# Kernel optimization log

Measured on AMD Instinct MI355X. Metric: run time of the kernel, lower is better.

Reference implementation:

```python
import jax, jax.numpy as jnp
import numpy as np

# ---- problem constants (mirror AdjustInstanceArea __init__ args) ----
NUM_NODES = 2_000_000
NUM_MOVABLE = 1_500_000
NUM_FILLER = 400_000
NUM_NETS = 1_500_000
PINS_PER_NET = 4                       # uniform netpin_start = arange(0, P+1, 4)
NUM_PINS = NUM_NETS * PINS_PER_NET
XL, XH, YL, YH = 0.0, 1000.0, 0.0, 1000.0
NBX = NBY = 512
BIN_W = (XH - XL) / NBX
BIN_H = (YH - YL) / NBY
UNIT_H_CAP = 1.5                       # unit horizontal routing capacity
UNIT_V_CAP = 1.5                       # unit vertical routing capacity
MAX_RATE = 2.0                         # max_route_opt_adjust_rate
MIN_RATE = 1.0 / MAX_RATE
EPS = 1e-6


def setup_inputs() -> dict:
    key = jax.random.key(0)
    k = jax.random.split(key, 4)
    x = jax.random.uniform(k[0], (NUM_NODES,), jnp.float32, XL, XH - 4.0)
    y = jax.random.uniform(k[1], (NUM_NODES,), jnp.float32, YL, YH - 4.0)
    pos = jnp.concatenate([x, y])                      # [2*num_nodes], x then y

    # pins clustered around net centers (realistic small net bboxes)
    rng = np.random.default_rng(0)
    centers = rng.uniform(0.0, 1000.0, size=(NUM_NETS, 1, 2)).astype(np.float32)
    jit = rng.uniform(-20.0, 20.0, size=(NUM_NETS, PINS_PER_NET, 2)).astype(np.float32)
    ppos = np.clip(centers + jit, 0.0, 1000.0)         # [nets, pins_per_net, 2], in net order

    # flat_netpin: pin ids grouped by net; pin_pos indexed by pin id
    flat_netpin = rng.permutation(NUM_PINS).astype(np.int32)
    px = np.empty(NUM_PINS, np.float32); py = np.empty(NUM_PINS, np.float32)
    px[flat_netpin] = ppos[..., 0].reshape(-1)
    py[flat_netpin] = ppos[..., 1].reshape(-1)
    pin_pos = jnp.concatenate([jnp.asarray(px), jnp.asarray(py)])  # [2*num_pins]

    pin2net = jnp.asarray(np.repeat(np.arange(NUM_NETS, dtype=np.int32), PINS_PER_NET))

    node_size_x = jax.random.uniform(k[2], (NUM_NODES,), jnp.float32, 1.0, 4.0)
    node_size_y = jax.random.uniform(k[3], (NUM_NODES,), jnp.float32, 1.0, 4.0)
    return {"pos": pos, "pin_pos": pin_pos,
            "node_size_x": node_size_x, "node_size_y": node_size_y,
            "flat_netpin": jnp.asarray(flat_netpin), "pin2net": pin2net}


def _rect_accum(vals, blx, bly, bhx, bhy):
    """Accumulate vals over inclusive bin rectangles via difference map + 2D cumsum."""
    D = jnp.zeros((NBX + 1, NBY + 1), vals.dtype)
    D = D.at[blx, bly].add(vals)
    D = D.at[bhx + 1, bly].add(-vals)
    D = D.at[blx, bhy + 1].add(-vals)
    D = D.at[bhx + 1, bhy + 1].add(vals)
    return jnp.cumsum(jnp.cumsum(D, axis=0), axis=1)[:NBX, :NBY]


def reference(pos, pin_pos, node_size_x, node_size_y, flat_netpin, pin2net):
    # ---- InstanceRouteOptimizationArea: RUDY routing demand per bin ----
    px = pin_pos[:NUM_PINS][flat_netpin].reshape(NUM_NETS, PINS_PER_NET)
    py = pin_pos[NUM_PINS:][flat_netpin].reshape(NUM_NETS, PINS_PER_NET)
    net_xl = jnp.min(px, axis=1); net_xh = jnp.max(px, axis=1)
    net_yl = jnp.min(py, axis=1); net_yh = jnp.max(py, axis=1)
    bw = net_xh - net_xl
    bh = net_yh - net_yl
    barea = jnp.maximum(bw * bh, EPS)
    dens_h = bw / barea                                # horizontal wire density
    dens_v = bh / barea                                # vertical wire density

    blx = jnp.clip(jnp.floor((net_xl - XL) / BIN_W), 0, NBX - 1).astype(jnp.int32)
    bhx = jnp.clip(jnp.floor((net_xh - XL) / BIN_W), 0, NBX - 1).astype(jnp.int32)
    bly = jnp.clip(jnp.floor((net_yl - YL) / BIN_H), 0, NBY - 1).astype(jnp.int32)
    bhy = jnp.clip(jnp.floor((net_yh - YL) / BIN_H), 0, NBY - 1).astype(jnp.int32)

    util_h = _rect_accum(dens_h, blx, bly, bhx, bhy) / UNIT_H_CAP
    util_v = _rect_accum(dens_v, blx, bly, bhx, bhy) / UNIT_V_CAP

    # per-movable-node utilization (gather at node center bin)
    x = pos[:NUM_NODES]; y = pos[NUM_NODES:]
    nsx_m = node_size_x[:NUM_MOVABLE]; nsy_m = node_size_y[:NUM_MOVABLE]
    cx = x[:NUM_MOVABLE] + 0.5 * nsx_m
    cy = y[:NUM_MOVABLE] + 0.5 * nsy_m
    bix = jnp.clip(jnp.floor((cx - XL) / BIN_W), 0, NBX - 1).astype(jnp.int32)
    biy = jnp.clip(jnp.floor((cy - YL) / BIN_H), 0, NBY - 1).astype(jnp.int32)
    util = jnp.maximum(util_h[bix, biy], util_v[bix, biy])
    ratio = jnp.clip(util, MIN_RATE, MAX_RATE)

    area_old = nsx_m * nsy_m
    instance_route_area = area_old * ratio

    # ---- AdjustInstanceArea: rescale under max_total_area budget ----
    filler_area_old = jnp.sum(node_size_x[NUM_NODES - NUM_FILLER:] *
                              node_size_y[NUM_NODES - NUM_FILLER:])
    max_total_area = jnp.sum(area_old) + filler_area_old
    scale = jnp.minimum(1.0, max_total_area / jnp.maximum(jnp.sum(instance_route_area), EPS))
    new_area = instance_route_area * scale
    sr = jnp.sqrt(new_area / jnp.maximum(area_old, EPS))
    nsx_new = nsx_m * sr
    nsy_new = nsy_m * sr

    # keep cell centers fixed while resizing
    x_out = x.at[:NUM_MOVABLE].add(0.5 * (nsx_m - nsx_new))
    y_out = y.at[:NUM_MOVABLE].add(0.5 * (nsy_m - nsy_new))

    # fillers absorb leftover area budget
    fscale = jnp.sqrt(jnp.maximum(max_total_area - jnp.sum(new_area), 0.0) /
                      jnp.maximum(filler_area_old, EPS))
    nsx_out = node_size_x.at[:NUM_MOVABLE].set(nsx_new)
    nsx_out = nsx_out.at[NUM_NODES - NUM_FILLER:].multiply(fscale)
    nsy_out = node_size_y.at[:NUM_MOVABLE].set(nsy_new)
    nsy_out = nsy_out.at[NUM_NODES - NUM_FILLER:].multiply(fscale)

    return jnp.concatenate([x_out, y_out, nsx_out, nsy_out])  # [4*num_nodes]
```

## Files before the change

### kernel.cpp

```cpp
#include <hip/hip_runtime.h>
#include <math.h>

#define N_NODES   2000000
#define N_MOVABLE 1500000
#define N_FILLER  400000
#define N_NETS    1500000
#define N_PINS    (N_NETS * 4)
#define NB        512
#define NT        16
#define TILE      32
#define NBUCKET   (NT * NT)
#define CAP       10240
#define RED_BLOCKS 512

__device__ __forceinline__ int bin_idx(float v) {
    float b = floorf(v / 1.953125f);
    b = fminf(fmaxf(b, 0.0f), 511.0f);
    return (int)b;
}

__global__ void pack_kernel(const float* __restrict__ pin_pos,
                            float2* __restrict__ pp) {
    int i = blockIdx.x * blockDim.x + threadIdx.x;
    if (i >= N_PINS / 4) return;
    float4 a = reinterpret_cast<const float4*>(pin_pos)[i];
    float4 b = reinterpret_cast<const float4*>(pin_pos + N_PINS)[i];
    float4* o = reinterpret_cast<float4*>(pp + 4 * (size_t)i);
    o[0] = make_float4(a.x, b.x, a.y, b.y);
    o[1] = make_float4(a.z, b.z, a.w, b.w);
}

template <bool PACKED>
__global__ __launch_bounds__(1024)
void gather_bin_kernel(const float* __restrict__ pin_pos,
                       const float2* __restrict__ pp,
                       const int*  __restrict__ flat_netpin,
                       float4* __restrict__ slab,
                       unsigned* __restrict__ g_ptr) {
    __shared__ unsigned hist[NBUCKET];
    __shared__ unsigned base[NBUCKET];
    int t = threadIdx.x;
    if (t < NBUCKET) hist[t] = 0;
    __syncthreads();

    int n = blockIdx.x * 1024 + t;
    float4 r = make_float4(0.f, 0.f, 0.f, 0.f);
    int b = 0;
    unsigned rank = 0;
    bool valid = (n < N_NETS);
    if (valid) {
        int4 fp = *reinterpret_cast<const int4*>(flat_netpin + 4 * n);
        float px0, px1, px2, px3, py0, py1, py2, py3;
        if (PACKED) {
            float2 p0 = pp[fp.x], p1 = pp[fp.y], p2 = pp[fp.z], p3 = pp[fp.w];
            px0 = p0.x; py0 = p0.y; px1 = p1.x; py1 = p1.y;
            px2 = p2.x; py2 = p2.y; px3 = p3.x; py3 = p3.y;
        } else {
            px0 = pin_pos[fp.x]; px1 = pin_pos[fp.y];
            px2 = pin_pos[fp.z]; px3 = pin_pos[fp.w];
            py0 = pin_pos[N_PINS + fp.x]; py1 = pin_pos[N_PINS + fp.y];
            py2 = pin_pos[N_PINS + fp.z]; py3 = pin_pos[N_PINS + fp.w];
        }
        float xl = fminf(fminf(px0, px1), fminf(px2, px3));
        float xh = fmaxf(fmaxf(px0, px1), fmaxf(px2, px3));
        float yl = fminf(fminf(py0, py1), fminf(py2, py3));
        float yh = fmaxf(fmaxf(py0, py1), fmaxf(py2, py3));

        float bw = xh - xl, bh = yh - yl;
        float barea = fmaxf(bw * bh, 1e-6f);
        float vh = (bw / barea) * (1.0f / 1.5f);
        float vv = (bh / barea) * (1.0f / 1.5f);

        unsigned blx = bin_idx(xl), bhx = bin_idx(xh);
        unsigned bly = bin_idx(yl), bhy = bin_idx(yh);

        r.x = vh; r.y = vv;
        r.z = __uint_as_float(blx | (bly << 16));
        r.w = __uint_as_float((bhx + 1) | ((bhy + 1) << 16));
        b = (int)((bly >> 5) * NT + (blx >> 5));
        rank = atomicAdd(&hist[b], 1u);
    }
    __syncthreads();
    if (t < NBUCKET) {
        unsigned c = hist[t];
        base[t] = c ? atomicAdd(&g_ptr[t], c) : 0u;
    }
    __syncthreads();
    if (valid) {
        unsigned slot = base[b] + rank;
        if (slot < CAP) slab[(size_t)b * CAP + slot] = r;
    }
}

__global__ __launch_bounds__(256)
void accum_kernel(const float4* __restrict__ slab,
                  const unsigned* __restrict__ g_cnt,
                  float2* __restrict__ Dp) {
    __shared__ float acc[TILE][TILE][2];
    int wg   = blockIdx.x;
    int half = wg & 1;
    int tile = wg >> 1;
    int tx = tile & (NT - 1);
    int ty = tile >> 4;

    for (int i = threadIdx.x; i < TILE * TILE * 2; i += 256)
        ((float*)acc)[i] = 0.0f;
    __syncthreads();

    int x0 = tx * TILE, y0 = ty * TILE;
    for (int dy = -1; dy <= 0; ++dy) {
        int sy = ty + dy; if (sy < 0) continue;
        for (int dx = -1; dx <= 0; ++dx) {
            int sx = tx + dx; if (sx < 0) continue;
            int sb = sy * NT + sx;
            unsigned cnt = min(g_cnt[sb], (unsigned)CAP);
            unsigned lo = half ? cnt / 2 : 0u;
            unsigned hi = half ? cnt : cnt / 2;
            const float4* recs = slab + (size_t)sb * CAP;
            for (unsigned i = lo + threadIdx.x; i < hi; i += 256) {
                float4 r = recs[i];
                unsigned zlo = __float_as_uint(r.z), zhi = __float_as_uint(r.w);
                int ax0 = (int)(zlo & 0xffffu), ay0 = (int)(zlo >> 16);
                int ax1 = (int)(zhi & 0xffffu), ay1 = (int)(zhi >> 16);
                int X0 = ax0 - x0, X1 = ax1 - x0;
                int Y0 = ay0 - y0, Y1 = ay1 - y0;
                bool inX0 = (unsigned)X0 < TILE, inX1 = (unsigned)X1 < TILE;
                bool inY0 = (unsigned)Y0 < TILE, inY1 = (unsigned)Y1 < TILE;
                if (inX0 && inY0) { atomicAdd(&acc[X0][Y0][0],  r.x); atomicAdd(&acc[X0][Y0][1],  r.y); }
                if (inX1 && inY0) { atomicAdd(&acc[X1][Y0][0], -r.x); atomicAdd(&acc[X1][Y0][1], -r.y); }
                if (inX0 && inY1) { atomicAdd(&acc[X0][Y1][0], -r.x); atomicAdd(&acc[X0][Y1][1], -r.y); }
                if (inX1 && inY1) { atomicAdd(&acc[X1][Y1][0],  r.x); atomicAdd(&acc[X1][Y1][1],  r.y); }
            }
        }
    }
    __syncthreads();
    float2* D = Dp + (size_t)half * NB * NB;
    for (int i = threadIdx.x; i < TILE * TILE; i += 256) {
        int X = i >> 5, Y = i & 31;
        D[(size_t)(x0 + X) * NB + (y0 + Y)] = make_float2(acc[X][Y][0], acc[X][Y][1]);
    }
}

__global__ void fb_scatter_kernel(const float4* __restrict__ rec,
                                  float2* __restrict__ Dp) {
    int n = blockIdx.x * blockDim.x + threadIdx.x;
    if (n >= N_NETS) return;
    float4 r = rec[n];
    unsigned zlo = __float_as_uint(r.z), zhi = __float_as_uint(r.w);
    int ax0 = (int)(zlo & 0xffffu), ay0 = (int)(zlo >> 16);
    int ax1 = (int)(zhi & 0xffffu), ay1 = (int)(zhi >> 16);
    if (ax0 < NB && ay0 < NB) { unsafeAtomicAdd(&Dp[ax0 * NB + ay0].x,  r.x); unsafeAtomicAdd(&Dp[ax0 * NB + ay0].y,  r.y); }
    if (ax1 < NB && ay0 < NB) { unsafeAtomicAdd(&Dp[ax1 * NB + ay0].x, -r.x); unsafeAtomicAdd(&Dp[ax1 * NB + ay0].y, -r.y); }
    if (ax0 < NB && ay1 < NB) { unsafeAtomicAdd(&Dp[ax0 * NB + ay1].x, -r.x); unsafeAtomicAdd(&Dp[ax0 * NB + ay1].y, -r.y); }
    if (ax1 < NB && ay1 < NB) { unsafeAtomicAdd(&Dp[ax1 * NB + ay1].x,  r.x); unsafeAtomicAdd(&Dp[ax1 * NB + ay1].y,  r.y); }
}

__global__ void scan_x_kernel(const float2* __restrict__ Dp,
                              float2* __restrict__ S) {
    __shared__ float2 s[NB];
    int y = blockIdx.x;
    int t = threadIdx.x;
    float2 a = Dp[(size_t)t * NB + y];
    float2 b = Dp[(size_t)NB * NB + (size_t)t * NB + y];
    s[t] = make_float2(a.x + b.x, a.y + b.y);
    __syncthreads();
    for (int off = 1; off < NB; off <<= 1) {
        float2 u = s[t];
        if (t >= off) { float2 w = s[t - off]; u.x += w.x; u.y += w.y; }
        __syncthreads();
        s[t] = u;
        __syncthreads();
    }
    S[(size_t)t * NB + y] = s[t];
}

__global__ void scan_y_kernel(float2* __restrict__ S) {
    __shared__ float2 s[NB];
    int x = blockIdx.x;
    int t = threadIdx.x;
    s[t] = S[(size_t)x * NB + t];
    __syncthreads();
    for (int off = 1; off < NB; off <<= 1) {
        float2 u = s[t];
        if (t >= off) { float2 w = s[t - off]; u.x += w.x; u.y += w.y; }
        __syncthreads();
        s[t] = u;
        __syncthreads();
    }
    S[(size_t)x * NB + t] = s[t];
}

__global__ void reduce_kernel(const float* __restrict__ pos,
                              const float* __restrict__ nsx,
                              const float* __restrict__ nsy,
                              const float2* __restrict__ S,
                              double* __restrict__ partials) {
    double a_old = 0.0, a_route = 0.0, a_fill = 0.0;
    int stride = gridDim.x * blockDim.x;
    for (int i = blockIdx.x * blockDim.x + threadIdx.x;
         i < N_MOVABLE + N_FILLER; i += stride) {
        if (i < N_MOVABLE) {
            float sx = nsx[i], sy = nsy[i];
            float cx = pos[i] + 0.5f * sx;
            float cy = pos[N_NODES + i] + 0.5f * sy;
            int bx = bin_idx(cx), by = bin_idx(cy);
            float2 u2 = S[(size_t)bx * NB + by];
            float ratio = fminf(fmaxf(fmaxf(u2.x, u2.y), 0.5f), 2.0f);
            float area = sx * sy;
            a_old += (double)area;
            a_route += (double)(area * ratio);
        } else {
            int j = (N_NODES - N_FILLER) + (i - N_MOVABLE);
            a_fill += (double)(nsx[j] * nsy[j]);
        }
    }
    for (int off = 32; off > 0; off >>= 1) {
        a_old   += __shfl_down(a_old, off);
        a_route += __shfl_down(a_route, off);
        a_fill  += __shfl_down(a_fill, off);
    }
    __shared__ double sd[4][3];
    int wid = threadIdx.x >> 6, lane = threadIdx.x & 63;
    if (lane == 0) { sd[wid][0] = a_old; sd[wid][1] = a_route; sd[wid][2] = a_fill; }
    __syncthreads();
    if (threadIdx.x == 0) {
        double s0 = 0, s1 = 0, s2 = 0;
        for (int w = 0; w < 4; ++w) { s0 += sd[w][0]; s1 += sd[w][1]; s2 += sd[w][2]; }
        partials[blockIdx.x * 3 + 0] = s0;
        partials[blockIdx.x * 3 + 1] = s1;
        partials[blockIdx.x * 3 + 2] = s2;
    }
}

__global__ void finish_kernel(const double* __restrict__ partials,
                              double* __restrict__ sums) {
    int t = threadIdx.x;
    double s0 = partials[t * 3 + 0];
    double s1 = partials[t * 3 + 1];
    double s2 = partials[t * 3 + 2];
    for (int off = 32; off > 0; off >>= 1) {
        s0 += __shfl_down(s0, off);
        s1 += __shfl_down(s1, off);
        s2 += __shfl_down(s2, off);
    }
    __shared__ double sd[8][3];
    int wid = t >> 6, lane = t & 63;
    if (lane == 0) { sd[wid][0] = s0; sd[wid][1] = s1; sd[wid][2] = s2; }
    __syncthreads();
    if (t == 0) {
        double a = 0, b = 0, c = 0;
        for (int w = 0; w < 8; ++w) { a += sd[w][0]; b += sd[w][1]; c += sd[w][2]; }
        sums[0] = a; sums[1] = b; sums[2] = c;
    }
}

__global__ void final_kernel(const float* __restrict__ pos,
                             const float* __restrict__ nsx,
                             const float* __restrict__ nsy,
                             const float2* __restrict__ S,
                             const double* __restrict__ sums,
                             float* __restrict__ out) {
    double sum_area  = sums[0];
    double sum_route = sums[1];
    double fill_old  = sums[2];
    double max_total = sum_area + fill_old;

    float scale = fminf(1.0f, (float)(max_total / fmax(sum_route, 1e-6)));
    float sum_new = (float)(scale * (float)sum_route);
    float fscale = sqrtf(fmaxf((float)max_total - sum_new, 0.0f) /
                         fmaxf((float)fill_old, 1e-6f));

    int stride = gridDim.x * blockDim.x;
    for (int i = blockIdx.x * blockDim.x + threadIdx.x; i < N_NODES; i += stride) {
        float x = pos[i], y = pos[N_NODES + i];
        float sx = nsx[i], sy = nsy[i];
        float ox = x, oy = y, osx = sx, osy = sy;

        if (i < N_MOVABLE) {
            float cx = x + 0.5f * sx;
            float cy = y + 0.5f * sy;
            int bx = bin_idx(cx), by = bin_idx(cy);
            float2 u2 = S[(size_t)bx * NB + by];
            float ratio = fminf(fmaxf(fmaxf(u2.x, u2.y), 0.5f), 2.0f);
            float area = sx * sy;
            float new_area = area * ratio * scale;
            float sr = sqrtf(new_area / fmaxf(area, 1e-6f));
            float sx_new = sx * sr, sy_new = sy * sr;
            ox = x + 0.5f * (sx - sx_new);
            oy = y + 0.5f * (sy - sy_new);
            osx = sx_new; osy = sy_new;
        } else if (i >= N_NODES - N_FILLER) {
            osx = sx * fscale;
            osy = sy * fscale;
        }

        out[i] = ox;
        out[N_NODES + i] = oy;
        out[2 * N_NODES + i] = osx;
        out[3 * N_NODES + i] = osy;
    }
}

extern "C" void kernel_launch(void* const* d_in, const int* in_sizes, int n_in,
                              void* d_out, int out_size, void* d_ws, size_t ws_size,
                              hipStream_t stream) {
    const float* pos         = (const float*)d_in[0];
    const float* pin_pos     = (const float*)d_in[1];
    const float* nsx         = (const float*)d_in[2];
    const float* nsy         = (const float*)d_in[3];
    const int*   flat_netpin = (const int*)d_in[4];
    float* out = (float*)d_out;

    const size_t pp_b   = (size_t)N_PINS * sizeof(float2);
    const size_t slab_b = (size_t)NBUCKET * CAP * sizeof(float4);
    const size_t dp_b   = (size_t)2 * NB * NB * sizeof(float2);
    const size_t s_b    = (size_t)NB * NB * sizeof(float2);
    const size_t gp_b   = (size_t)NBUCKET * sizeof(unsigned);
    const size_t part_b = (size_t)RED_BLOCKS * 3 * sizeof(double);
    const size_t sums_b = 32;

    const size_t need_base = slab_b + dp_b + s_b + gp_b + part_b + sums_b;
    const size_t need_full = need_base + pp_b;

    bool use_slab = (ws_size >= need_base);
    bool packed   = (ws_size >= need_full);

    char* base = (char*)d_ws;
    float2* pp = nullptr;
    if (packed) { pp = (float2*)base; base += pp_b; }
    float4*   slab     = (float4*)base;   base += slab_b;
    float2*   Dp       = (float2*)base;   base += dp_b;
    float2*   S        = (float2*)base;   base += s_b;
    unsigned* g_ptr    = (unsigned*)base; base += gp_b;
    double*   partials = (double*)base;   base += part_b;
    double*   sums     = (double*)base;

    if (use_slab) {
        hipMemsetAsync(g_ptr, 0, gp_b, stream);
        const int GB_BLOCKS = (N_NETS + 1023) / 1024;
        if (packed) {
            pack_kernel<<<(N_PINS / 4 + 255) / 256, 256, 0, stream>>>(pin_pos, pp);
            gather_bin_kernel<true><<<GB_BLOCKS, 1024, 0, stream>>>(pin_pos, pp, flat_netpin, slab, g_ptr);
        } else {
            gather_bin_kernel<false><<<GB_BLOCKS, 1024, 0, stream>>>(pin_pos, pp, flat_netpin, slab, g_ptr);
        }
        accum_kernel<<<2 * NBUCKET, 256, 0, stream>>>(slab, g_ptr, Dp);
    } else {
        hipMemsetAsync(Dp, 0, dp_b, stream);
        gather_bin_kernel<false><<<(N_NETS + 1023) / 1024, 1024, 0, stream>>>(
            pin_pos, nullptr, flat_netpin, slab, g_ptr);
        fb_scatter_kernel<<<(N_NETS + 255) / 256, 256, 0, stream>>>(slab, Dp);
    }

    scan_x_kernel<<<NB, NB, 0, stream>>>(Dp, S);
    scan_y_kernel<<<NB, NB, 0, stream>>>(S);

    reduce_kernel<<<RED_BLOCKS, 256, 0, stream>>>(pos, nsx, nsy, S, partials);
    finish_kernel<<<1, 512, 0, stream>>>(partials, sums);
    final_kernel<<<(N_NODES + 255) / 256, 256, 0, stream>>>(pos, nsx, nsy, S, sums, out);
}
```

Baseline: 253.4 us.

## Accumulate each bucket once into 64x64 halo tiles, vectorize node kernels, alias workspace

```diff
diff --git a/kernel.cpp b/kernel.cpp
--- a/kernel.cpp
+++ b/kernel.cpp
@@ -11,7 +11,9 @@
 #define TILE      32
 #define NBUCKET   (NT * NT)
 #define CAP       10240
+#define NMAPS     8
 #define RED_BLOCKS 512
+#define NPB       2048
 
 __device__ __forceinline__ int bin_idx(float v) {
     float b = floorf(v / 1.953125f);
@@ -31,10 +33,41 @@
 }
 
 template <bool PACKED>
+__device__ __forceinline__ float4 make_rec(const float* __restrict__ pin_pos,
+                                           const float2* __restrict__ pp,
+                                           int4 fp, int* bucket) {
+    float2 p0, p1, p2, p3;
+    if (PACKED) {
+        p0 = pp[fp.x]; p1 = pp[fp.y]; p2 = pp[fp.z]; p3 = pp[fp.w];
+    } else {
+        p0 = make_float2(pin_pos[fp.x], pin_pos[N_PINS + fp.x]);
+        p1 = make_float2(pin_pos[fp.y], pin_pos[N_PINS + fp.y]);
+        p2 = make_float2(pin_pos[fp.z], pin_pos[N_PINS + fp.z]);
+        p3 = make_float2(pin_pos[fp.w], pin_pos[N_PINS + fp.w]);
+    }
+    float xl = fminf(fminf(p0.x, p1.x), fminf(p2.x, p3.x));
+    float xh = fmaxf(fmaxf(p0.x, p1.x), fmaxf(p2.x, p3.x));
+    float yl = fminf(fminf(p0.y, p1.y), fminf(p2.y, p3.y));
+    float yh = fmaxf(fmaxf(p0.y, p1.y), fmaxf(p2.y, p3.y));
+    float bw = xh - xl, bh = yh - yl;
+    float barea = fmaxf(bw * bh, 1e-6f);
+    float vh = (bw / barea) * (1.0f / 1.5f);
+    float vv = (bh / barea) * (1.0f / 1.5f);
+    unsigned blx = bin_idx(xl), bhx = bin_idx(xh);
+    unsigned bly = bin_idx(yl), bhy = bin_idx(yh);
+    *bucket = (int)((bly >> 5) * NT + (blx >> 5));
+    float4 r;
+    r.x = vh; r.y = vv;
+    r.z = __uint_as_float(blx | (bly << 16));
+    r.w = __uint_as_float((bhx + 1) | ((bhy + 1) << 16));
+    return r;
+}
+
+template <bool PACKED>
 __global__ __launch_bounds__(1024)
 void gather_bin_kernel(const float* __restrict__ pin_pos,
                        const float2* __restrict__ pp,
-                       const int*  __restrict__ flat_netpin,
+                       const int*  __restrict__ fnp,
                        float4* __restrict__ slab,
                        unsigned* __restrict__ g_ptr) {
     __shared__ unsigned hist[NBUCKET];
@@ -43,126 +76,81 @@
     if (t < NBUCKET) hist[t] = 0;
     __syncthreads();
 
-    int n = blockIdx.x * 1024 + t;
-    float4 r = make_float4(0.f, 0.f, 0.f, 0.f);
-    int b = 0;
-    unsigned rank = 0;
-    bool valid = (n < N_NETS);
-    if (valid) {
-        int4 fp = *reinterpret_cast<const int4*>(flat_netpin + 4 * n);
-        float px0, px1, px2, px3, py0, py1, py2, py3;
-        if (PACKED) {
-            float2 p0 = pp[fp.x], p1 = pp[fp.y], p2 = pp[fp.z], p3 = pp[fp.w];
-            px0 = p0.x; py0 = p0.y; px1 = p1.x; py1 = p1.y;
-            px2 = p2.x; py2 = p2.y; px3 = p3.x; py3 = p3.y;
-        } else {
-            px0 = pin_pos[fp.x]; px1 = pin_pos[fp.y];
-            px2 = pin_pos[fp.z]; px3 = pin_pos[fp.w];
-            py0 = pin_pos[N_PINS + fp.x]; py1 = pin_pos[N_PINS + fp.y];
-            py2 = pin_pos[N_PINS + fp.z]; py3 = pin_pos[N_PINS + fp.w];
-        }
-        float xl = fminf(fminf(px0, px1), fminf(px2, px3));
-        float xh = fmaxf(fmaxf(px0, px1), fmaxf(px2, px3));
-        float yl = fminf(fminf(py0, py1), fminf(py2, py3));
-        float yh = fmaxf(fmaxf(py0, py1), fmaxf(py2, py3));
-
-        float bw = xh - xl, bh = yh - yl;
-        float barea = fmaxf(bw * bh, 1e-6f);
-        float vh = (bw / barea) * (1.0f / 1.5f);
-        float vv = (bh / barea) * (1.0f / 1.5f);
-
-        unsigned blx = bin_idx(xl), bhx = bin_idx(xh);
-        unsigned bly = bin_idx(yl), bhy = bin_idx(yh);
-
-        r.x = vh; r.y = vv;
-        r.z = __uint_as_float(blx | (bly << 16));
-        r.w = __uint_as_float((bhx + 1) | ((bhy + 1) << 16));
-        b = (int)((bly >> 5) * NT + (blx >> 5));
-        rank = atomicAdd(&hist[b], 1u);
-    }
+    int n0 = blockIdx.x * NPB + t;
+    int n1 = n0 + 1024;
+    bool v0 = (n0 < N_NETS), v1 = (n1 < N_NETS);
+
+    int4 fpA = v0 ? *reinterpret_cast<const int4*>(fnp + 4 * (size_t)n0) : make_int4(0,0,0,0);
+    int4 fpB = v1 ? *reinterpret_cast<const int4*>(fnp + 4 * (size_t)n1) : make_int4(0,0,0,0);
+
+    float4 r0, r1; int b0 = 0, b1 = 0; unsigned rk0 = 0, rk1 = 0;
+    if (v0) { r0 = make_rec<PACKED>(pin_pos, pp, fpA, &b0); rk0 = atomicAdd(&hist[b0], 1u); }
+    if (v1) { r1 = make_rec<PACKED>(pin_pos, pp, fpB, &b1); rk1 = atomicAdd(&hist[b1], 1u); }
     __syncthreads();
     if (t < NBUCKET) {
         unsigned c = hist[t];
         base[t] = c ? atomicAdd(&g_ptr[t], c) : 0u;
     }
     __syncthreads();
-    if (valid) {
-        unsigned slot = base[b] + rank;
-        if (slot < CAP) slab[(size_t)b * CAP + slot] = r;
-    }
+    if (v0) { unsigned s = base[b0] + rk0; if (s < CAP) slab[(size_t)b0 * CAP + s] = r0; }
+    if (v1) { unsigned s = base[b1] + rk1; if (s < CAP) slab[(size_t)b1 * CAP + s] = r1; }
 }
 
 __global__ __launch_bounds__(256)
 void accum_kernel(const float4* __restrict__ slab,
                   const unsigned* __restrict__ g_cnt,
                   float2* __restrict__ Dp) {
-    __shared__ float acc[TILE][TILE][2];
-    int wg   = blockIdx.x;
-    int half = wg & 1;
-    int tile = wg >> 1;
-    int tx = tile & (NT - 1);
-    int ty = tile >> 4;
-
-    for (int i = threadIdx.x; i < TILE * TILE * 2; i += 256)
-        ((float*)acc)[i] = 0.0f;
+    __shared__ float2 acc[64 * 64];
+    int wg = blockIdx.x;
+    int h = wg & 1, tile = wg >> 1;
+    int tx = tile & (NT - 1), ty = tile >> 4;
+
+    for (int i = threadIdx.x; i < 64 * 64; i += 256) acc[i] = make_float2(0.f, 0.f);
     __syncthreads();
 
     int x0 = tx * TILE, y0 = ty * TILE;
-    for (int dy = -1; dy <= 0; ++dy) {
-        int sy = ty + dy; if (sy < 0) continue;
-        for (int dx = -1; dx <= 0; ++dx) {
-            int sx = tx + dx; if (sx < 0) continue;
-            int sb = sy * NT + sx;
-            unsigned cnt = min(g_cnt[sb], (unsigned)CAP);
-            unsigned lo = half ? cnt / 2 : 0u;
-            unsigned hi = half ? cnt : cnt / 2;
-            const float4* recs = slab + (size_t)sb * CAP;
-            for (unsigned i = lo + threadIdx.x; i < hi; i += 256) {
-                float4 r = recs[i];
-                unsigned zlo = __float_as_uint(r.z), zhi = __float_as_uint(r.w);
-                int ax0 = (int)(zlo & 0xffffu), ay0 = (int)(zlo >> 16);
-                int ax1 = (int)(zhi & 0xffffu), ay1 = (int)(zhi >> 16);
-                int X0 = ax0 - x0, X1 = ax1 - x0;
-                int Y0 = ay0 - y0, Y1 = ay1 - y0;
-                bool inX0 = (unsigned)X0 < TILE, inX1 = (unsigned)X1 < TILE;
-                bool inY0 = (unsigned)Y0 < TILE, inY1 = (unsigned)Y1 < TILE;
-                if (inX0 && inY0) { atomicAdd(&acc[X0][Y0][0],  r.x); atomicAdd(&acc[X0][Y0][1],  r.y); }
-                if (inX1 && inY0) { atomicAdd(&acc[X1][Y0][0], -r.x); atomicAdd(&acc[X1][Y0][1], -r.y); }
-                if (inX0 && inY1) { atomicAdd(&acc[X0][Y1][0], -r.x); atomicAdd(&acc[X0][Y1][1], -r.y); }
-                if (inX1 && inY1) { atomicAdd(&acc[X1][Y1][0],  r.x); atomicAdd(&acc[X1][Y1][1],  r.y); }
-            }
-        }
-    }
-    __syncthreads();
-    float2* D = Dp + (size_t)half * NB * NB;
-    for (int i = threadIdx.x; i < TILE * TILE; i += 256) {
-        int X = i >> 5, Y = i & 31;
-        D[(size_t)(x0 + X) * NB + (y0 + Y)] = make_float2(acc[X][Y][0], acc[X][Y][1]);
-    }
-}
-
-__global__ void fb_scatter_kernel(const float4* __restrict__ rec,
-                                  float2* __restrict__ Dp) {
-    int n = blockIdx.x * blockDim.x + threadIdx.x;
-    if (n >= N_NETS) return;
-    float4 r = rec[n];
-    unsigned zlo = __float_as_uint(r.z), zhi = __float_as_uint(r.w);
-    int ax0 = (int)(zlo & 0xffffu), ay0 = (int)(zlo >> 16);
-    int ax1 = (int)(zhi & 0xffffu), ay1 = (int)(zhi >> 16);
-    if (ax0 < NB && ay0 < NB) { unsafeAtomicAdd(&Dp[ax0 * NB + ay0].x,  r.x); unsafeAtomicAdd(&Dp[ax0 * NB + ay0].y,  r.y); }
-    if (ax1 < NB && ay0 < NB) { unsafeAtomicAdd(&Dp[ax1 * NB + ay0].x, -r.x); unsafeAtomicAdd(&Dp[ax1 * NB + ay0].y, -r.y); }
-    if (ax0 < NB && ay1 < NB) { unsafeAtomicAdd(&Dp[ax0 * NB + ay1].x, -r.x); unsafeAtomicAdd(&Dp[ax0 * NB + ay1].y, -r.y); }
-    if (ax1 < NB && ay1 < NB) { unsafeAtomicAdd(&Dp[ax1 * NB + ay1].x,  r.x); unsafeAtomicAdd(&Dp[ax1 * NB + ay1].y,  r.y); }
-}
-
-__global__ void scan_x_kernel(const float2* __restrict__ Dp,
-                              float2* __restrict__ S) {
+    unsigned cnt = min(g_cnt[tile], (unsigned)CAP);
+    unsigned lo = h ? cnt / 2 : 0u;
+    unsigned hi = h ? cnt : cnt / 2;
+    const float4* recs = slab + (size_t)tile * CAP;
+
+    for (unsigned i = lo + threadIdx.x; i < hi; i += 256) {
+        float4 r = recs[i];
+        unsigned zlo = __float_as_uint(r.z), zhi = __float_as_uint(r.w);
+        int ax0 = (int)(zlo & 0xffffu), ay0 = (int)(zlo >> 16);
+        int ax1 = (int)(zhi & 0xffffu), ay1 = (int)(zhi >> 16);
+        int X0 = ax0 - x0, Y0 = ay0 - y0;
+        int X1 = ax1 - x0, Y1 = ay1 - y0;
+        bool okx1 = (ax1 < NB), oky1 = (ay1 < NB);
+        atomicAdd(&acc[X0 * 64 + Y0].x,  r.x);
+        atomicAdd(&acc[X0 * 64 + Y0].y,  r.y);
+        if (okx1) { atomicAdd(&acc[X1 * 64 + Y0].x, -r.x); atomicAdd(&acc[X1 * 64 + Y0].y, -r.y); }
+        if (oky1) { atomicAdd(&acc[X0 * 64 + Y1].x, -r.x); atomicAdd(&acc[X0 * 64 + Y1].y, -r.y); }
+        if (okx1 && oky1) { atomicAdd(&acc[X1 * 64 + Y1].x, r.x); atomicAdd(&acc[X1 * 64 + Y1].y, r.y); }
+    }
+    __syncthreads();
+
+    int m = h * 4 + (ty & 1) * 2 + (tx & 1);
+    float2* D = Dp + (size_t)m * NB * NB;
+    for (int i = threadIdx.x; i < 64 * 64; i += 256) {
+        int X = i >> 6, Y = i & 63;
+        int gx = x0 + X, gy = y0 + Y;
+        if (gx < NB && gy < NB) D[(size_t)gx * NB + gy] = acc[i];
+    }
+}
+
+__global__ void scanA_kernel(const float2* __restrict__ Dp,
+                             float2* __restrict__ S) {
     __shared__ float2 s[NB];
-    int y = blockIdx.x;
-    int t = threadIdx.x;
-    float2 a = Dp[(size_t)t * NB + y];
-    float2 b = Dp[(size_t)NB * NB + (size_t)t * NB + y];
-    s[t] = make_float2(a.x + b.x, a.y + b.y);
+    int x = blockIdx.x, t = threadIdx.x;
+    float2 a = make_float2(0.f, 0.f);
+    #pragma unroll
+    for (int m = 0; m < NMAPS; ++m) {
+        if (((m & 1) && x < TILE) || ((m & 2) && t < TILE)) continue;
+        float2 v = Dp[(size_t)m * NB * NB + (size_t)x * NB + t];
+        a.x += v.x; a.y += v.y;
+    }
+    s[t] = a;
     __syncthreads();
     for (int off = 1; off < NB; off <<= 1) {
         float2 u = s[t];
@@ -171,14 +159,13 @@
         s[t] = u;
         __syncthreads();
     }
-    S[(size_t)t * NB + y] = s[t];
-}
-
-__global__ void scan_y_kernel(float2* __restrict__ S) {
+    S[(size_t)x * NB + t] = s[t];
+}
+
+__global__ void scanB_kernel(float2* __restrict__ S) {
     __shared__ float2 s[NB];
-    int x = blockIdx.x;
-    int t = threadIdx.x;
-    s[t] = S[(size_t)x * NB + t];
+    int y = blockIdx.x, t = threadIdx.x;
+    s[t] = S[(size_t)t * NB + y];
     __syncthreads();
     for (int off = 1; off < NB; off <<= 1) {
         float2 u = s[t];
@@ -187,31 +174,46 @@
         s[t] = u;
         __syncthreads();
     }
-    S[(size_t)x * NB + t] = s[t];
-}
-
-__global__ void reduce_kernel(const float* __restrict__ pos,
-                              const float* __restrict__ nsx,
-                              const float* __restrict__ nsy,
-                              const float2* __restrict__ S,
-                              double* __restrict__ partials) {
+    S[(size_t)t * NB + y] = s[t];
+}
+
+__global__ __launch_bounds__(256)
+void reduce_kernel(const float* __restrict__ pos,
+                   const float* __restrict__ nsx,
+                   const float* __restrict__ nsy,
+                   const float2* __restrict__ S,
+                   double* __restrict__ partials) {
+    const int MQ = N_MOVABLE / 4;
+    const int TQ = MQ + N_FILLER / 4;
     double a_old = 0.0, a_route = 0.0, a_fill = 0.0;
     int stride = gridDim.x * blockDim.x;
-    for (int i = blockIdx.x * blockDim.x + threadIdx.x;
-         i < N_MOVABLE + N_FILLER; i += stride) {
-        if (i < N_MOVABLE) {
-            float sx = nsx[i], sy = nsy[i];
-            float cx = pos[i] + 0.5f * sx;
-            float cy = pos[N_NODES + i] + 0.5f * sy;
-            int bx = bin_idx(cx), by = bin_idx(cy);
-            float2 u2 = S[(size_t)bx * NB + by];
-            float ratio = fminf(fmaxf(fmaxf(u2.x, u2.y), 0.5f), 2.0f);
-            float area = sx * sy;
-            a_old += (double)area;
-            a_route += (double)(area * ratio);
+    for (int q = blockIdx.x * blockDim.x + threadIdx.x; q < TQ; q += stride) {
+        if (q < MQ) {
+            int i = 4 * q;
+            float4 x4  = *reinterpret_cast<const float4*>(pos + i);
+            float4 y4  = *reinterpret_cast<const float4*>(pos + N_NODES + i);
+            float4 sx4 = *reinterpret_cast<const float4*>(nsx + i);
+            float4 sy4 = *reinterpret_cast<const float4*>(nsy + i);
+            float xs[4] = {x4.x, x4.y, x4.z, x4.w};
+            float ys[4] = {y4.x, y4.y, y4.z, y4.w};
+            float sxs[4] = {sx4.x, sx4.y, sx4.z, sx4.w};
+            float sys[4] = {sy4.x, sy4.y, sy4.z, sy4.w};
+            #pragma unroll
+            for (int k = 0; k < 4; ++k) {
+                int bx = bin_idx(xs[k] + 0.5f * sxs[k]);
+                int by = bin_idx(ys[k] + 0.5f * sys[k]);
+                float2 u2 = S[(size_t)bx * NB + by];
+                float ratio = fminf(fmaxf(fmaxf(u2.x, u2.y), 0.5f), 2.0f);
+                float area = sxs[k] * sys[k];
+                a_old += (double)area;
+                a_route += (double)(area * ratio);
+            }
         } else {
-            int j = (N_NODES - N_FILLER) + (i - N_MOVABLE);
-            a_fill += (double)(nsx[j] * nsy[j]);
+            int j = (N_NODES - N_FILLER) + 4 * (q - MQ);
+            float4 sx4 = *reinterpret_cast<const float4*>(nsx + j);
+            float4 sy4 = *reinterpret_cast<const float4*>(nsy + j);
+            a_fill += (double)(sx4.x * sy4.x + sx4.y * sy4.y +
+                               sx4.z * sy4.z + sx4.w * sy4.w);
         }
     }
     for (int off = 32; off > 0; off >>= 1) {
@@ -254,12 +256,13 @@
     }
 }
 
-__global__ void final_kernel(const float* __restrict__ pos,
-                             const float* __restrict__ nsx,
-                             const float* __restrict__ nsy,
-                             const float2* __restrict__ S,
-                             const double* __restrict__ sums,
-                             float* __restrict__ out) {
+__global__ __launch_bounds__(256)
+void final_kernel(const float* __restrict__ pos,
+                  const float* __restrict__ nsx,
+                  const float* __restrict__ nsy,
+                  const float2* __restrict__ S,
+                  const double* __restrict__ sums,
+                  float* __restrict__ out) {
     double sum_area  = sums[0];
     double sum_route = sums[1];
     double fill_old  = sums[2];
@@ -270,35 +273,44 @@
     float fscale = sqrtf(fmaxf((float)max_total - sum_new, 0.0f) /
                          fmaxf((float)fill_old, 1e-6f));
 
-    int stride = gridDim.x * blockDim.x;
-    for (int i = blockIdx.x * blockDim.x + threadIdx.x; i < N_NODES; i += stride) {
-        float x = pos[i], y = pos[N_NODES + i];
-        float sx = nsx[i], sy = nsy[i];
-        float ox = x, oy = y, osx = sx, osy = sy;
-
-        if (i < N_MOVABLE) {
-            float cx = x + 0.5f * sx;
-            float cy = y + 0.5f * sy;
-            int bx = bin_idx(cx), by = bin_idx(cy);
+    int q = blockIdx.x * blockDim.x + threadIdx.x;
+    if (q >= N_NODES / 4) return;
+    int i = 4 * q;
+
+    float4 x4  = *reinterpret_cast<const float4*>(pos + i);
+    float4 y4  = *reinterpret_cast<const float4*>(pos + N_NODES + i);
+    float4 sx4 = *reinterpret_cast<const float4*>(nsx + i);
+    float4 sy4 = *reinterpret_cast<const float4*>(nsy + i);
+
+    float xs[4] = {x4.x, x4.y, x4.z, x4.w};
+    float ys[4] = {y4.x, y4.y, y4.z, y4.w};
+    float sxs[4] = {sx4.x, sx4.y, sx4.z, sx4.w};
+    float sys[4] = {sy4.x, sy4.y, sy4.z, sy4.w};
+
+    if (i < N_MOVABLE) {
+        #pragma unroll
+        for (int k = 0; k < 4; ++k) {
+            int bx = bin_idx(xs[k] + 0.5f * sxs[k]);
+            int by = bin_idx(ys[k] + 0.5f * sys[k]);
             float2 u2 = S[(size_t)bx * NB + by];
             float ratio = fminf(fmaxf(fmaxf(u2.x, u2.y), 0.5f), 2.0f);
-            float area = sx * sy;
+            float area = sxs[k] * sys[k];
             float new_area = area * ratio * scale;
             float sr = sqrtf(new_area / fmaxf(area, 1e-6f));
-            float sx_new = sx * sr, sy_new = sy * sr;
-            ox = x + 0.5f * (sx - sx_new);
-            oy = y + 0.5f * (sy - sy_new);
-            osx = sx_new; osy = sy_new;
-        } else if (i >= N_NODES - N_FILLER) {
-            osx = sx * fscale;
-            osy = sy * fscale;
+            float sx_new = sxs[k] * sr, sy_new = sys[k] * sr;
+            xs[k] = xs[k] + 0.5f * (sxs[k] - sx_new);
+            ys[k] = ys[k] + 0.5f * (sys[k] - sy_new);
+            sxs[k] = sx_new; sys[k] = sy_new;
         }
-
-        out[i] = ox;
-        out[N_NODES + i] = oy;
-        out[2 * N_NODES + i] = osx;
-        out[3 * N_NODES + i] = osy;
-    }
+    } else if (i >= N_NODES - N_FILLER) {
+        #pragma unroll
+        for (int k = 0; k < 4; ++k) { sxs[k] *= fscale; sys[k] *= fscale; }
+    }
+
+    *reinterpret_cast<float4*>(out + i)               = make_float4(xs[0], xs[1], xs[2], xs[3]);
+    *reinterpret_cast<float4*>(out + N_NODES + i)     = make_float4(ys[0], ys[1], ys[2], ys[3]);
+    *reinterpret_cast<float4*>(out + 2 * N_NODES + i) = make_float4(sxs[0], sxs[1], sxs[2], sxs[3]);
+    *reinterpret_cast<float4*>(out + 3 * N_NODES + i) = make_float4(sys[0], sys[1], sys[2], sys[3]);
 }
 
 extern "C" void kernel_launch(void* const* d_in, const int* in_sizes, int n_in,
@@ -313,49 +325,50 @@
 
     const size_t pp_b   = (size_t)N_PINS * sizeof(float2);
     const size_t slab_b = (size_t)NBUCKET * CAP * sizeof(float4);
-    const size_t dp_b   = (size_t)2 * NB * NB * sizeof(float2);
+    const size_t dp_b   = (size_t)NMAPS * NB * NB * sizeof(float2);
     const size_t s_b    = (size_t)NB * NB * sizeof(float2);
-    const size_t gp_b   = (size_t)NBUCKET * sizeof(unsigned);
     const size_t part_b = (size_t)RED_BLOCKS * 3 * sizeof(double);
-    const size_t sums_b = 32;
-
-    const size_t need_base = slab_b + dp_b + s_b + gp_b + part_b + sums_b;
-    const size_t need_full = need_base + pp_b;
-
-    bool use_slab = (ws_size >= need_base);
-    bool packed   = (ws_size >= need_full);
-
+    const size_t gp_b   = 4096;
+
+    const size_t need_primary = pp_b + slab_b + gp_b + 64;
+
+    float2* pp = nullptr;
+    float4* slab; float2* Dp; float2* S; double* partials;
+    unsigned* g_ptr; double* sums;
     char* base = (char*)d_ws;
-    float2* pp = nullptr;
-    if (packed) { pp = (float2*)base; base += pp_b; }
-    float4*   slab     = (float4*)base;   base += slab_b;
-    float2*   Dp       = (float2*)base;   base += dp_b;
-    float2*   S        = (float2*)base;   base += s_b;
-    unsigned* g_ptr    = (unsigned*)base; base += gp_b;
-    double*   partials = (double*)base;   base += part_b;
-    double*   sums     = (double*)base;
-
-    if (use_slab) {
-        hipMemsetAsync(g_ptr, 0, gp_b, stream);
-        const int GB_BLOCKS = (N_NETS + 1023) / 1024;
-        if (packed) {
-            pack_kernel<<<(N_PINS / 4 + 255) / 256, 256, 0, stream>>>(pin_pos, pp);
-            gather_bin_kernel<true><<<GB_BLOCKS, 1024, 0, stream>>>(pin_pos, pp, flat_netpin, slab, g_ptr);
-        } else {
-            gather_bin_kernel<false><<<GB_BLOCKS, 1024, 0, stream>>>(pin_pos, pp, flat_netpin, slab, g_ptr);
-        }
-        accum_kernel<<<2 * NBUCKET, 256, 0, stream>>>(slab, g_ptr, Dp);
+    bool packed = (ws_size >= need_primary);
+    if (packed) {
+        pp       = (float2*)base;
+        Dp       = (float2*)base;
+        S        = (float2*)(base + dp_b);
+        partials = (double*)(base + dp_b + s_b);
+        slab     = (float4*)(base + pp_b);
+        g_ptr    = (unsigned*)(base + pp_b + slab_b);
+        sums     = (double*)(base + pp_b + slab_b + gp_b);
     } else {
-        hipMemsetAsync(Dp, 0, dp_b, stream);
-        gather_bin_kernel<false><<<(N_NETS + 1023) / 1024, 1024, 0, stream>>>(
-            pin_pos, nullptr, flat_netpin, slab, g_ptr);
-        fb_scatter_kernel<<<(N_NETS + 255) / 256, 256, 0, stream>>>(slab, Dp);
-    }
-
-    scan_x_kernel<<<NB, NB, 0, stream>>>(Dp, S);
-    scan_y_kernel<<<NB, NB, 0, stream>>>(S);
+        slab     = (float4*)base;
+        Dp       = (float2*)(base + slab_b);
+        S        = (float2*)(base + slab_b + dp_b);
+        partials = (double*)(base + slab_b + dp_b + s_b);
+        g_ptr    = (unsigned*)(base + slab_b + dp_b + s_b + part_b);
+        sums     = (double*)((char*)g_ptr + gp_b);
+    }
+
+    hipMemsetAsync(g_ptr, 0, NBUCKET * sizeof(unsigned), stream);
+
+    const int GB_BLOCKS = (N_NETS + NPB - 1) / NPB;
+    if (packed) {
+        pack_kernel<<<(N_PINS / 4 + 255) / 256, 256, 0, stream>>>(pin_pos, pp);
+        gather_bin_kernel<true><<<GB_BLOCKS, 1024, 0, stream>>>(pin_pos, pp, flat_netpin, slab, g_ptr);
+    } else {
+        gather_bin_kernel<false><<<GB_BLOCKS, 1024, 0, stream>>>(pin_pos, nullptr, flat_netpin, slab, g_ptr);
+    }
+
+    accum_kernel<<<2 * NBUCKET, 256, 0, stream>>>(slab, g_ptr, Dp);
+    scanA_kernel<<<NB, NB, 0, stream>>>(Dp, S);
+    scanB_kernel<<<NB, NB, 0, stream>>>(S);
 
     reduce_kernel<<<RED_BLOCKS, 256, 0, stream>>>(pos, nsx, nsy, S, partials);
     finish_kernel<<<1, 512, 0, stream>>>(partials, sums);
-    final_kernel<<<(N_NODES + 255) / 256, 256, 0, stream>>>(pos, nsx, nsy, S, sums, out);
-}
+    final_kernel<<<(N_NODES / 4 + 255) / 256, 256, 0, stream>>>(pos, nsx, nsy, S, sums, out);
+}
```

Result: slower. 267.9 us (+5.7%).
